# Optimization experiments

Hardware: AMD Instinct MI355X
Metric: run time of the kernel (lower is better)

Reference implementation:

```python
import jax, jax.numpy as jnp
import numpy as np

EPS = 1e-8  # torch F.cosine_similarity eps


def setup_inputs() -> dict:
    key = jax.random.key(0)
    k1, k2 = jax.random.split(key)
    N, D, F = 2048, 128, 8
    out_matrix = jax.random.normal(k1, (2, N, D, F), dtype=jnp.float32)
    label_matrix = jax.random.uniform(k2, (F, N, N), dtype=jnp.float32)
    margin = jnp.float32(0.1)
    return {"out_matrix": out_matrix, "label_matrix": label_matrix,
            "margin": margin, "sample_num": N}


def _cosine_sim(q, d):
    # q, d: [F, N, D] -> [F, N, N]
    dots = jnp.einsum('fqd,fkd->fqk', q, d)
    nq = jnp.linalg.norm(q, axis=-1)  # [F, N]
    nd = jnp.linalg.norm(d, axis=-1)
    denom = jnp.maximum(nq[:, :, None] * nd[:, None, :], EPS)
    return dots / denom


def reference(out_matrix, label_matrix, margin, sample_num):
    # out_matrix: [2, N, D, F]; label_matrix: [F, N, N]
    q = jnp.transpose(out_matrix[0], (2, 0, 1))  # [F, N, D] query per index slice
    d = jnp.transpose(out_matrix[1], (2, 0, 1))  # [F, N, D] document per index slice
    sim = _cosine_sim(q, d)                      # [F, N, N]

    # accuracy: argmax over rows vs label argmax
    correction_num = jnp.sum(jnp.argmax(sim, axis=2) == jnp.argmax(label_matrix, axis=2))

    # pairwise max-margin hinge: t1[i,j] = sim[i,i]-sim[i,j], t2 likewise for labels
    diag_s = jnp.diagonal(sim, axis1=1, axis2=2)            # [F, N]
    diag_l = jnp.diagonal(label_matrix, axis1=1, axis2=2)   # [F, N]
    t1 = diag_s[:, :, None] - sim
    t2 = diag_l[:, :, None] - label_matrix
    loss_mat = margin - t1 * t2                             # [F, N, N]
    N = sim.shape[1]
    off_diag = 1.0 - jnp.eye(N, dtype=loss_mat.dtype)       # zero the diagonal
    loss = jnp.sum(jnp.maximum(loss_mat * off_diag, 0.0))
    return (loss, correction_num)
```

## Files before the change

kernel.cpp:

```cpp
#include <hip/hip_runtime.h>
#include <hip/hip_bf16.h>

static constexpr int N = 2048;
static constexpr int D = 128;
static constexpr int F = 8;
static constexpr int RS = 256;

static constexpr size_t OFF_LOSS = 0;
static constexpr size_t OFF_CNT  = 4;
static constexpr size_t OFF_PSIM = 1024;
static constexpr size_t OFF_PLAB = 1024 + 2097152;
static constexpr size_t OFF_RNQ  = OFF_PLAB + 2097152;
static constexpr size_t OFF_RND  = OFF_RNQ + 65536;
static constexpr size_t OFF_DIAGS= OFF_RND + 65536;
static constexpr size_t OFF_DIAGL= OFF_DIAGS + 65536;
static constexpr size_t OFF_QC   = OFF_DIAGL + 65536;
static constexpr size_t OFF_DC   = OFF_QC + (size_t)F * N * RS * 2;

typedef __attribute__((ext_vector_type(8))) short short8;
typedef __attribute__((ext_vector_type(4))) float f32x4;
typedef unsigned long long u64;

__device__ __forceinline__ unsigned fmap(float x) {
    unsigned u = __float_as_uint(x);
    return (u & 0x80000000u) ? ~u : (u | 0x80000000u);
}
__device__ __forceinline__ float bf2f(ushort u) { return __uint_as_float(((unsigned)u) << 16); }
__device__ __forceinline__ ushort f2bf(float x) {
    __hip_bfloat16 h = __float2bfloat16(x);
    return *(ushort*)&h;
}
__device__ __forceinline__ void gload_lds16(const void* g, void* l) {
    __builtin_amdgcn_global_load_lds(
        (const __attribute__((address_space(1))) void*)g,
        (__attribute__((address_space(3))) void*)l, 16, 0, 0);
}

__global__ __launch_bounds__(256) void pack_kernel(
    const float* __restrict__ om, const float* __restrict__ label,
    ushort* __restrict__ Qc, ushort* __restrict__ Dc,
    float* __restrict__ rnq, float* __restrict__ rnd,
    float* __restrict__ diag_s, float* __restrict__ diag_l) {
    __shared__ float buf[4][1152];
    const int i0 = blockIdx.x * 2;
    const int t = threadIdx.x;
#pragma unroll
    for (int s = 0; s < 4; s++) {
        const int r2 = s >> 1, side = s & 1;
        float4 v = *(const float4*)(om + ((size_t)side * N + i0 + r2) * (D * F) + t * 4);
#pragma unroll
        for (int e = 0; e < 4; e++) {
            int g = t * 4 + e;
            buf[s][(g >> 3) * 9 + (g & 7)] = ((const float*)&v)[e];
        }
    }
    __syncthreads();
    const int r2 = t >> 7, f = (t >> 4) & 7, k8 = t & 15;
    float v0[8], v1[8];
#pragma unroll
    for (int j = 0; j < 8; j++) {
        v0[j] = buf[r2 * 2 + 0][(k8 * 8 + j) * 9 + f];
        v1[j] = buf[r2 * 2 + 1][(k8 * 8 + j) * 9 + f];
    }
    short8 H0, L0, H1, L1;
    float s0 = 0.f, s1 = 0.f, p = 0.f;
#pragma unroll
    for (int j = 0; j < 8; j++) {
        ushort h0 = f2bf(v0[j]); ushort l0 = f2bf(v0[j] - bf2f(h0));
        ushort h1 = f2bf(v1[j]); ushort l1 = f2bf(v1[j] - bf2f(h1));
        H0[j] = (short)h0; L0[j] = (short)l0; H1[j] = (short)h1; L1[j] = (short)l1;
        s0 += v0[j] * v0[j]; s1 += v1[j] * v1[j]; p += v0[j] * v1[j];
    }
    const int i = i0 + r2;
    const size_t base = ((size_t)f * N + i) * RS + k8 * 8;
    *(short8*)&Qc[base]       = H0;
    *(short8*)&Qc[base + 128] = L0;
    *(short8*)&Dc[base]       = H1;
    *(short8*)&Dc[base + 128] = L1;
#pragma unroll
    for (int off = 1; off < 16; off <<= 1) {
        s0 += __shfl_xor(s0, off, 64);
        s1 += __shfl_xor(s1, off, 64);
        p  += __shfl_xor(p,  off, 64);
    }
    if (k8 == 0) {
        float rq = 1.0f / sqrtf(s0), rd = 1.0f / sqrtf(s1);
        rnq[f * N + i] = rq;
        rnd[f * N + i] = rd;
        diag_s[f * N + i] = p * rq * rd;
        diag_l[f * N + i] = label[((size_t)f * N + i) * N + i];
    }
}

__global__ __launch_bounds__(256, 4) void main_kernel(
    const ushort* __restrict__ Qc, const ushort* __restrict__ Dc,
    const float* __restrict__ label,
    const float* __restrict__ rnq, const float* __restrict__ rnd,
    const float* __restrict__ diag_s, const float* __restrict__ diag_l,
    const float* __restrict__ marginp,
    u64* __restrict__ psim, u64* __restrict__ plab,
    float* __restrict__ loss_acc) {
    __shared__ __align__(16) char smem[34816];
    ushort* As = (ushort*)smem;
    ushort* Bs = (ushort*)(smem + 16384);
    u64* kbS = (u64*)smem;
    u64* kbL = (u64*)(smem + 17408);
    __shared__ float lred[4];

    const int f = blockIdx.z;
    const int i0 = blockIdx.y * 128;
    const int j0 = blockIdx.x * 128;
    const int t = threadIdx.x;
    const int lane = t & 63, wave = t >> 6;
    const int lhi = lane >> 4, llo = lane & 15;

    f32x4 acc[2][8];
#pragma unroll
    for (int a = 0; a < 2; a++)
#pragma unroll
        for (int b = 0; b < 8; b++) acc[a][b] = (f32x4){0.f, 0.f, 0.f, 0.f};

    const char* Ag = (const char*)(Qc + ((size_t)f * N + i0) * RS);
    const char* Bg = (const char*)(Dc + ((size_t)f * N + j0) * RS);
    char* AsB = smem;
    char* BsB = smem + 16384;
    const int srow = t >> 3, schunk = t & 7;
    const int qo[6]    = {0, 128, 0, 128, 256, 384};
    const int doffs[6] = {0, 128, 256, 384, 0, 128};

#pragma unroll
    for (int it = 0; it < 6; it++) {
#pragma unroll
        for (int p = 0; p < 4; p++) {
            const int row = srow + p * 32;
            const int gc = schunk ^ (row & 7);
            gload_lds16(Ag + (size_t)row * 512 + qo[it] + gc * 16, AsB + t * 16 + p * 4096);
            gload_lds16(Bg + (size_t)row * 512 + doffs[it] + gc * 16, BsB + t * 16 + p * 4096);
        }
        __syncthreads();
#pragma unroll
        for (int kk = 0; kk < 64; kk += 32) {
            const int kc = kk >> 3;
            short8 af[2], bfv[8];
#pragma unroll
            for (int a = 0; a < 2; a++) {
                const int R = wave * 32 + a * 16 + llo;
                af[a] = *(const short8*)&As[R * 64 + (((kc + lhi) ^ (R & 7)) * 8)];
            }
#pragma unroll
            for (int b = 0; b < 8; b++) {
                const int R = b * 16 + llo;
                bfv[b] = *(const short8*)&Bs[R * 64 + (((kc + lhi) ^ (R & 7)) * 8)];
            }
#pragma unroll
            for (int a = 0; a < 2; a++)
#pragma unroll
                for (int b = 0; b < 8; b++)
                    acc[a][b] = __builtin_amdgcn_mfma_f32_16x16x32_bf16(af[a], bfv[b], acc[a][b], 0, 0, 0);
        }
        __syncthreads();
    }

    const float margin = *marginp;
    float loss = 0.f;
    float rdl[8];
#pragma unroll
    for (int b = 0; b < 8; b++) rdl[b] = rnd[f * N + j0 + b * 16 + llo];

#pragma unroll
    for (int a = 0; a < 2; a++) {
#pragma unroll
        for (int reg = 0; reg < 4; reg++) {
            const int rloc = wave * 32 + a * 16 + lhi * 4 + reg;
            const int i = i0 + rloc;
            const float rq = rnq[f * N + i];
            const float ds = diag_s[f * N + i];
            const float dl = diag_l[f * N + i];
            const float* lrow = label + ((size_t)f * N + i) * N + j0;
            u64 bestS = 0ull, bestL = 0ull;
#pragma unroll
            for (int b = 0; b < 8; b++) {
                const int j = j0 + b * 16 + llo;
                const float sim = acc[a][b][reg] * rq * rdl[b];
                const float lb = lrow[b * 16 + llo];
                const float lm = margin - (ds - sim) * (dl - lb);
                loss += (j != i && lm > 0.f) ? lm : 0.f;
                u64 ks = (((u64)fmap(sim)) << 32) | (u64)(0xFFFFFFFFu - (unsigned)j);
                u64 kl = (((u64)fmap(lb)) << 32) | (u64)(0xFFFFFFFFu - (unsigned)j);
                bestS = (ks > bestS) ? ks : bestS;
                bestL = (kl > bestL) ? kl : bestL;
            }
            kbS[rloc * 17 + llo] = bestS;
            kbL[rloc * 17 + llo] = bestL;
        }
    }
    __syncthreads();
    {
        const int r = t & 127;
        const u64* kb = (t < 128) ? kbS : kbL;
        u64 best = 0ull;
#pragma unroll
        for (int k = 0; k < 16; k++) {
            u64 v = kb[r * 17 + k];
            best = (v > best) ? v : best;
        }
        u64* dst = (t < 128) ? psim : plab;
        dst[(size_t)blockIdx.x * (F * N) + f * N + i0 + r] = best;
    }

    for (int off = 32; off >= 1; off >>= 1) loss += __shfl_down(loss, off, 64);
    if ((t & 63) == 0) lred[t >> 6] = loss;
    __syncthreads();
    if (t == 0) atomicAdd(loss_acc, lred[0] + lred[1] + lred[2] + lred[3]);
}

__global__ __launch_bounds__(256) void reduce_kernel(
    const u64* __restrict__ psim, const u64* __restrict__ plab, int* __restrict__ cnt) {
    const int r = blockIdx.x * 256 + threadIdx.x;
    u64 bs = 0ull, bl = 0ull;
#pragma unroll
    for (int jb = 0; jb < 16; jb++) {
        u64 v = psim[(size_t)jb * (F * N) + r]; bs = (v > bs) ? v : bs;
        u64 w = plab[(size_t)jb * (F * N) + r]; bl = (w > bl) ? w : bl;
    }
    int c = ((unsigned)(bs & 0xFFFFFFFFull) == (unsigned)(bl & 0xFFFFFFFFull)) ? 1 : 0;
    for (int off = 32; off >= 1; off >>= 1) c += __shfl_down(c, off, 64);
    __shared__ int cred[4];
    if ((threadIdx.x & 63) == 0) cred[threadIdx.x >> 6] = c;
    __syncthreads();
    if (threadIdx.x == 0) atomicAdd(cnt, cred[0] + cred[1] + cred[2] + cred[3]);
}

__global__ void write_kernel(const float* __restrict__ loss_acc,
                             const int* __restrict__ cnt, float* __restrict__ out) {
    out[0] = *loss_acc;
    out[1] = (float)(*cnt);
}

extern "C" void kernel_launch(void* const* d_in, const int* in_sizes, int n_in,
                              void* d_out, int out_size, void* d_ws, size_t ws_size,
                              hipStream_t stream) {
    const float* om     = (const float*)d_in[0];
    const float* label  = (const float*)d_in[1];
    const float* margin = (const float*)d_in[2];
    (void)in_sizes; (void)n_in; (void)out_size; (void)ws_size;

    char* ws = (char*)d_ws;
    float* loss_acc = (float*)(ws + OFF_LOSS);
    int*   cnt      = (int*)(ws + OFF_CNT);
    u64*   psim     = (u64*)(ws + OFF_PSIM);
    u64*   plab     = (u64*)(ws + OFF_PLAB);
    float* rnq    = (float*)(ws + OFF_RNQ);
    float* rnd    = (float*)(ws + OFF_RND);
    float* diag_s = (float*)(ws + OFF_DIAGS);
    float* diag_l = (float*)(ws + OFF_DIAGL);
    ushort* Qc    = (ushort*)(ws + OFF_QC);
    ushort* Dc    = (ushort*)(ws + OFF_DC);

    hipMemsetAsync(ws, 0, 8, stream);

    pack_kernel<<<N / 2, 256, 0, stream>>>(om, label, Qc, Dc, rnq, rnd, diag_s, diag_l);

    dim3 grid(N / 128, N / 128, F);
    main_kernel<<<grid, 256, 0, stream>>>(Qc, Dc, label, rnq, rnd, diag_s, diag_l,
                                          margin, psim, plab, loss_acc);

    reduce_kernel<<<F * N / 256, 256, 0, stream>>>(psim, plab, cnt);
    write_kernel<<<1, 1, 0, stream>>>(loss_acc, cnt, (float*)d_out);
}
```

Before: 255.0 us.

## Switch to 32x32x16 MFMA tiles with shuffle-based row argmax reduction

Replaces the 16x16x32 bf16 MFMA tiling (2x8 accumulators per wave) with 32x32x16 MFMA (4 accumulators of 16 floats), which changes the fragment-to-row/column mapping throughout the epilogue. The per-row argmax is now reduced across the 32 column lanes with xor shuffles instead of staging partial maxima through shared memory and a second pass. Row norms, diagonals and column norms are preloaded into shared memory once per block. This aims to cut LDS fragment loads per MFMA and remove the epilogue LDS round trip and barrier, at the cost of more shuffle instructions and a different register layout.

Measured after the change: 322.0 us. 26.3% more time.

```diff
diff --git a/kernel.cpp b/kernel.cpp
--- a/kernel.cpp
+++ b/kernel.cpp
@@ -18,7 +18,7 @@
 static constexpr size_t OFF_DC   = OFF_QC + (size_t)F * N * RS * 2;
 
 typedef __attribute__((ext_vector_type(8))) short short8;
-typedef __attribute__((ext_vector_type(4))) float f32x4;
+typedef __attribute__((ext_vector_type(16))) float f32x16;
 typedef unsigned long long u64;
 
 __device__ __forceinline__ unsigned fmap(float x) {
@@ -100,33 +100,42 @@
     const float* __restrict__ marginp,
     u64* __restrict__ psim, u64* __restrict__ plab,
     float* __restrict__ loss_acc) {
-    __shared__ __align__(16) char smem[34816];
+    __shared__ __align__(16) char smem[32768];
+    __shared__ float rowq[128], rowds[128], rowdl[128], colrd[128];
+    __shared__ float lred[4];
     ushort* As = (ushort*)smem;
     ushort* Bs = (ushort*)(smem + 16384);
-    u64* kbS = (u64*)smem;
-    u64* kbL = (u64*)(smem + 17408);
-    __shared__ float lred[4];
 
     const int f = blockIdx.z;
     const int i0 = blockIdx.y * 128;
     const int j0 = blockIdx.x * 128;
     const int t = threadIdx.x;
     const int lane = t & 63, wave = t >> 6;
-    const int lhi = lane >> 4, llo = lane & 15;
-
-    f32x4 acc[2][8];
-#pragma unroll
-    for (int a = 0; a < 2; a++)
-#pragma unroll
-        for (int b = 0; b < 8; b++) acc[a][b] = (f32x4){0.f, 0.f, 0.f, 0.f};
-
-    const char* Ag = (const char*)(Qc + ((size_t)f * N + i0) * RS);
-    const char* Bg = (const char*)(Dc + ((size_t)f * N + j0) * RS);
+    const int col = lane & 31, half = lane >> 5;
+    const int fN = f * N;
+
+    if (t < 128) {
+        rowq[t]  = rnq[fN + i0 + t];
+        rowds[t] = diag_s[fN + i0 + t];
+        rowdl[t] = diag_l[fN + i0 + t];
+    } else {
+        colrd[t - 128] = rnd[fN + j0 + t - 128];
+    }
+
+    f32x16 acc[4];
+#pragma unroll
+    for (int b = 0; b < 4; b++)
+#pragma unroll
+        for (int e = 0; e < 16; e++) acc[b][e] = 0.f;
+
+    const char* Ag = (const char*)(Qc + ((size_t)fN + i0) * RS);
+    const char* Bg = (const char*)(Dc + ((size_t)fN + j0) * RS);
     char* AsB = smem;
     char* BsB = smem + 16384;
     const int srow = t >> 3, schunk = t & 7;
     const int qo[6]    = {0, 128, 0, 128, 256, 384};
     const int doffs[6] = {0, 128, 256, 384, 0, 128};
+    const int sw = col & 7;
 
 #pragma unroll
     for (int it = 0; it < 6; it++) {
@@ -139,73 +148,61 @@
         }
         __syncthreads();
 #pragma unroll
-        for (int kk = 0; kk < 64; kk += 32) {
-            const int kc = kk >> 3;
-            short8 af[2], bfv[8];
-#pragma unroll
-            for (int a = 0; a < 2; a++) {
-                const int R = wave * 32 + a * 16 + llo;
-                af[a] = *(const short8*)&As[R * 64 + (((kc + lhi) ^ (R & 7)) * 8)];
+        for (int ks = 0; ks < 4; ks++) {
+            const int ck = ks * 2 + half;
+            const int Ra = wave * 32 + col;
+            short8 a = *(const short8*)&As[Ra * 64 + ((ck ^ sw) * 8)];
+            short8 bf[4];
+#pragma unroll
+            for (int b = 0; b < 4; b++) {
+                const int Rb = b * 32 + col;
+                bf[b] = *(const short8*)&Bs[Rb * 64 + ((ck ^ sw) * 8)];
             }
 #pragma unroll
-            for (int b = 0; b < 8; b++) {
-                const int R = b * 16 + llo;
-                bfv[b] = *(const short8*)&Bs[R * 64 + (((kc + lhi) ^ (R & 7)) * 8)];
-            }
-#pragma unroll
-            for (int a = 0; a < 2; a++)
-#pragma unroll
-                for (int b = 0; b < 8; b++)
-                    acc[a][b] = __builtin_amdgcn_mfma_f32_16x16x32_bf16(af[a], bfv[b], acc[a][b], 0, 0, 0);
+            for (int b = 0; b < 4; b++)
+                acc[b] = __builtin_amdgcn_mfma_f32_32x32x16_bf16(a, bf[b], acc[b], 0, 0, 0);
         }
         __syncthreads();
     }
 
     const float margin = *marginp;
     float loss = 0.f;
-    float rdl[8];
-#pragma unroll
-    for (int b = 0; b < 8; b++) rdl[b] = rnd[f * N + j0 + b * 16 + llo];
-
-#pragma unroll
-    for (int a = 0; a < 2; a++) {
-#pragma unroll
-        for (int reg = 0; reg < 4; reg++) {
-            const int rloc = wave * 32 + a * 16 + lhi * 4 + reg;
-            const int i = i0 + rloc;
-            const float rq = rnq[f * N + i];
-            const float ds = diag_s[f * N + i];
-            const float dl = diag_l[f * N + i];
-            const float* lrow = label + ((size_t)f * N + i) * N + j0;
-            u64 bestS = 0ull, bestL = 0ull;
-#pragma unroll
-            for (int b = 0; b < 8; b++) {
-                const int j = j0 + b * 16 + llo;
-                const float sim = acc[a][b][reg] * rq * rdl[b];
-                const float lb = lrow[b * 16 + llo];
-                const float lm = margin - (ds - sim) * (dl - lb);
-                loss += (j != i && lm > 0.f) ? lm : 0.f;
-                u64 ks = (((u64)fmap(sim)) << 32) | (u64)(0xFFFFFFFFu - (unsigned)j);
-                u64 kl = (((u64)fmap(lb)) << 32) | (u64)(0xFFFFFFFFu - (unsigned)j);
-                bestS = (ks > bestS) ? ks : bestS;
-                bestL = (kl > bestL) ? kl : bestL;
-            }
-            kbS[rloc * 17 + llo] = bestS;
-            kbL[rloc * 17 + llo] = bestL;
-        }
-    }
-    __syncthreads();
-    {
-        const int r = t & 127;
-        const u64* kb = (t < 128) ? kbS : kbL;
-        u64 best = 0ull;
-#pragma unroll
-        for (int k = 0; k < 16; k++) {
-            u64 v = kb[r * 17 + k];
-            best = (v > best) ? v : best;
-        }
-        u64* dst = (t < 128) ? psim : plab;
-        dst[(size_t)blockIdx.x * (F * N) + f * N + i0 + r] = best;
+    float rdl[4];
+#pragma unroll
+    for (int b = 0; b < 4; b++) rdl[b] = colrd[b * 32 + col];
+
+#pragma unroll
+    for (int reg = 0; reg < 16; reg++) {
+        const int rloc = wave * 32 + (reg & 3) + 8 * (reg >> 2) + 4 * half;
+        const int i = i0 + rloc;
+        const float rq = rowq[rloc];
+        const float ds = rowds[rloc];
+        const float dl = rowdl[rloc];
+        const float* lrow = label + ((size_t)fN + i) * N + j0;
+        u64 bestS = 0ull, bestL = 0ull;
+#pragma unroll
+        for (int b = 0; b < 4; b++) {
+            const int j = j0 + b * 32 + col;
+            const float sim = acc[b][reg] * rq * rdl[b];
+            const float lb = lrow[b * 32 + col];
+            const float lm = margin - (ds - sim) * (dl - lb);
+            loss += (j != i && lm > 0.f) ? lm : 0.f;
+            u64 ks = (((u64)fmap(sim)) << 32) | (u64)(0xFFFFFFFFu - (unsigned)j);
+            u64 kl = (((u64)fmap(lb)) << 32) | (u64)(0xFFFFFFFFu - (unsigned)j);
+            bestS = (ks > bestS) ? ks : bestS;
+            bestL = (kl > bestL) ? kl : bestL;
+        }
+#pragma unroll
+        for (int off = 1; off <= 16; off <<= 1) {
+            u64 oS = __shfl_xor(bestS, off, 64);
+            u64 oL = __shfl_xor(bestL, off, 64);
+            bestS = (oS > bestS) ? oS : bestS;
+            bestL = (oL > bestL) ? oL : bestL;
+        }
+        if (col == 0) {
+            psim[(size_t)blockIdx.x * (F * N) + fN + i] = bestS;
+            plab[(size_t)blockIdx.x * (F * N) + fN + i] = bestL;
+        }
     }
 
     for (int off = 32; off >= 1; off >>= 1) loss += __shfl_down(loss, off, 64);
```
